# Kernel optimization log

Hardware: AMD Instinct MI355X
Metric: run time of the kernel (lower is better)

Reference implementation:

```python
import jax, jax.numpy as jnp
import numpy as np

E, M, K, INTER = 8, 4096, 2048, 5632
N = 2 * INTER  # gate + up projections fused in w1
TOPK = 2


def setup_inputs() -> dict:
    key = jax.random.key(0)
    k1, k2, k3, k4, k5 = jax.random.split(key, 5)
    a1 = jax.random.normal(k1, (M, K), dtype=jnp.float32)
    w1 = jax.random.normal(k2, (E, N, K), dtype=jnp.float32) * (K ** -0.5)
    w2 = jax.random.normal(k3, (E, K, INTER), dtype=jnp.float32) * (INTER ** -0.5)
    topk_weights = jax.random.uniform(k4, (M, TOPK), dtype=jnp.float32)
    topk_ids = jax.random.randint(k5, (M, TOPK), 0, E, dtype=jnp.int64)
    return {"a1": a1, "w1": w1, "w2": w2,
            "topk_weights": topk_weights, "topk_ids": topk_ids}


def reference(a1, w1, w2, topk_weights, topk_ids):
    # Fused MoE: dispatch (identity/unquantized path) -> per-expert
    # SwiGLU expert GEMMs -> weighted combine over top-k routing.
    n_half = w1.shape[1] // 2
    fused = jnp.zeros((a1.shape[0], topk_ids.shape[1], w2.shape[1]), a1.dtype)  # [M, topk, K]
    for e in range(w1.shape[0]):  # small fixed expert count
        h = jnp.einsum('mk,nk->mn', a1, w1[e])          # [M, N]
        act = jax.nn.silu(h[:, :n_half]) * h[:, n_half:]  # [M, N/2]
        o = jnp.einsum('mn,kn->mk', act, w2[e])          # [M, K]
        mask = (topk_ids == e).astype(a1.dtype)          # [M, topk]
        fused = fused + mask[..., None] * o[:, None, :]
    # combine: weighted reduction over topk -> output [M, K]
    return jnp.einsum('mt,mtk->mk', topk_weights, fused)
```

## Files before the change

### kernel.cpp

```cpp
#include <hip/hip_runtime.h>
#include <hip/hip_bf16.h>

#define NEXP   8
#define MTOK   4096
#define KDIM   2048
#define NINTER 5632
#define NPAIR  8192

#define AS3 __attribute__((address_space(3)))
#define AS1 __attribute__((address_space(1)))

typedef __attribute__((ext_vector_type(4))) float f32x4;
typedef __attribute__((ext_vector_type(8))) short s16x8;

__device__ __forceinline__ short f2bf(float f) {
  union { float f; unsigned u; } v; v.f = f;
  unsigned r = v.u + 0x7FFFu + ((v.u >> 16) & 1u);
  return (short)(r >> 16);
}

__device__ __forceinline__ s16x8 pack8(float4 a, float4 b) {
  s16x8 v;
  v[0] = f2bf(a.x); v[1] = f2bf(a.y); v[2] = f2bf(a.z); v[3] = f2bf(a.w);
  v[4] = f2bf(b.x); v[5] = f2bf(b.y); v[6] = f2bf(b.z); v[7] = f2bf(b.w);
  return v;
}

#define N8_A1  ((size_t)MTOK * KDIM / 8)
#define N8_W1  ((size_t)NEXP * 2 * NINTER * KDIM / 8)
__global__ __launch_bounds__(256) void routecvt_k(const int* __restrict__ ids,
                                                  int* __restrict__ off,
                                                  int* __restrict__ list,
                                                  const float* __restrict__ a1,
                                                  unsigned short* __restrict__ a1b,
                                                  const float* __restrict__ w1,
                                                  unsigned short* __restrict__ w1b) {
  int tid = threadIdx.x;
  if (blockIdx.x == 0) {
    __shared__ int sids[NPAIR];
    __shared__ int scnt[64][8];
    __shared__ int sstart[64][8];
    __shared__ int s_is64;
    if (tid == 0) s_is64 = 1;
    __syncthreads();
    for (int i = tid; i < NPAIR / 2; i += 256)
      if (ids[2 * i + 1] != 0) s_is64 = 0;
    __syncthreads();
    int is64 = s_is64;
    for (int i = tid; i < NPAIR; i += 256) {
      int e = is64 ? ids[2 * i] : ids[i];
      if (e < 0) e = 0; if (e > 7) e = 7;
      sids[i] = e;
    }
    if (tid < 64)
      for (int e = 0; e < 8; ++e) scnt[tid][e] = 0;
    __syncthreads();
    if (tid < 64) {
      int b0 = tid * 128;
      for (int i = 0; i < 128; ++i) ++scnt[tid][sids[b0 + i]];
    }
    __syncthreads();
    if (tid == 0) {
      int tot = 0;
      for (int e = 0; e < 8; ++e) {
        off[e] = tot;
        for (int c = 0; c < 64; ++c) { sstart[c][e] = tot; tot += scnt[c][e]; }
      }
      off[8] = tot;
    }
    __syncthreads();
    if (tid < 64) {
      int b0 = tid * 128;
      for (int i = 0; i < 128; ++i) {
        int p = b0 + i;
        int e = sids[p];
        list[sstart[tid][e]++] = p;
      }
    }
  }
  size_t i = (size_t)blockIdx.x * 256 + tid;
  size_t stride = (size_t)gridDim.x * 256;
  for (; i < N8_A1 + N8_W1; i += stride) {
    if (i < N8_A1) {
      const float4* p = (const float4*)(a1 + i * 8);
      float4 f0 = p[0], f1 = p[1];
      *(s16x8*)(a1b + i * 8) = pack8(f0, f1);
    } else {
      size_t j = i - N8_A1;
      const float4* p = (const float4*)(w1 + j * 8);
      float4 f0 = p[0], f1 = p[1];
      *(s16x8*)(w1b + j * 8) = pack8(f0, f1);
    }
  }
}

template <int BF>
__global__ __launch_bounds__(256, 2) void gemm1_t(const float* __restrict__ a1,
                                                  const unsigned short* __restrict__ a1b,
                                                  const float* __restrict__ w1,
                                                  const unsigned short* __restrict__ w1b,
                                                  const float* __restrict__ w2f,
                                                  unsigned short* __restrict__ w2b,
                                                  const int* __restrict__ off,
                                                  const int* __restrict__ list,
                                                  unsigned short* __restrict__ act) {
  int e = blockIdx.z, mt = blockIdx.y, nt = blockIdx.x;
  int tid = threadIdx.x;

  if constexpr (BF) {
    if (mt >= 64) {
      const size_t N8_W2 = (size_t)NEXP * KDIM * NINTER / 8;
      size_t ci = (size_t)nt + 44u * ((mt - 64) + 9u * e);
      size_t g0 = ci * 3642 + tid;
      size_t end = (ci + 1) * 3642;
      if (end > N8_W2) end = N8_W2;
      for (size_t g = g0; g < end; g += 256) {
        const float4* s = (const float4*)(w2f + g * 8);
        float4 f0 = s[0], f1 = s[1];
        *(s16x8*)(w2b + g * 8) = pack8(f0, f1);
      }
      return;
    }
  }

  int base = off[e];
  int cnt  = off[e + 1] - base;
  if (mt * 128 >= cnt) return;
  __shared__ __align__(16) short lA[128 * 64];
  __shared__ __align__(16) short lBg[128 * 64];
  __shared__ __align__(16) short lBu[128 * 64];
  __shared__ int srow[128];
  if (tid < 128) {
    int r = mt * 128 + tid;
    srow[tid] = (r < cnt) ? (list[base + r] >> 1) : 0;
  }
  __syncthreads();
  int lane = tid & 63, wave = tid >> 6;
  int wm = wave >> 1, wn = wave & 1;
  int lrow = lane & 15, lhi = lane >> 4;
  f32x4 accg[4][4], accu[4][4];
#pragma unroll
  for (int i = 0; i < 4; ++i)
#pragma unroll
    for (int j = 0; j < 4; ++j) { accg[i][j] = (f32x4)(0.f); accu[i][j] = (f32x4)(0.f); }
  int n0 = nt * 128;

  const unsigned short* aSrc[4];
  const unsigned short* gSrc[4];
  const unsigned short* uSrc[4];
  if constexpr (BF) {
    const unsigned short* w1be = w1b + (size_t)e * (2 * NINTER) * KDIM;
    int c = lane & 7;
#pragma unroll
    for (int q = 0; q < 4; ++q) {
      int r = wave * 32 + q * 8 + (lane >> 3);
      int swz = (c ^ (r & 7)) * 8;
      aSrc[q] = a1b + (size_t)srow[r] * KDIM + swz;
      gSrc[q] = w1be + (size_t)(n0 + r) * KDIM + swz;
      uSrc[q] = w1be + (size_t)(NINTER + n0 + r) * KDIM + swz;
    }
  }
  const float* w1e = w1 + (size_t)e * (2 * NINTER) * KDIM;

  for (int k0 = 0; k0 < KDIM; k0 += 64) {
    if constexpr (BF) {
#pragma unroll
      for (int q = 0; q < 4; ++q) {
        int row0 = wave * 32 + q * 8;
        __builtin_amdgcn_global_load_lds((const AS1 void*)(aSrc[q] + k0), (AS3 void*)&lA[row0 * 64], 16, 0, 0);
        __builtin_amdgcn_global_load_lds((const AS1 void*)(gSrc[q] + k0), (AS3 void*)&lBg[row0 * 64], 16, 0, 0);
        __builtin_amdgcn_global_load_lds((const AS1 void*)(uSrc[q] + k0), (AS3 void*)&lBu[row0 * 64], 16, 0, 0);
      }
    } else {
#pragma unroll
      for (int c4 = 0; c4 < 4; ++c4) {
        int cid = c4 * 256 + tid;
        int row = cid >> 3, k8 = cid & 7;
        const float* s = a1 + (size_t)srow[row] * KDIM + k0 + k8 * 8;
        float4 f0 = *(const float4*)s;
        float4 f1 = *(const float4*)(s + 4);
        *(s16x8*)&lA[row * 64 + ((k8 ^ (row & 7)) * 8)] = pack8(f0, f1);
      }
#pragma unroll
      for (int c4 = 0; c4 < 4; ++c4) {
        int cid = c4 * 256 + tid;
        int row = cid >> 3, k8 = cid & 7;
        const float* sg = w1e + (size_t)(n0 + row) * KDIM + k0 + k8 * 8;
        const float* su = w1e + (size_t)(NINTER + n0 + row) * KDIM + k0 + k8 * 8;
        float4 g0 = *(const float4*)sg;
        float4 g1 = *(const float4*)(sg + 4);
        float4 u0 = *(const float4*)su;
        float4 u1 = *(const float4*)(su + 4);
        int o = row * 64 + ((k8 ^ (row & 7)) * 8);
        *(s16x8*)&lBg[o] = pack8(g0, g1);
        *(s16x8*)&lBu[o] = pack8(u0, u1);
      }
    }
    __syncthreads();
#pragma unroll
    for (int kk = 0; kk < 2; ++kk) {
      s16x8 af[4], bg[4], bu[4];
      int chunk = kk * 4 + lhi;
#pragma unroll
      for (int i = 0; i < 4; ++i) {
        int r = wm * 64 + i * 16 + lrow;
        af[i] = *(const s16x8*)&lA[r * 64 + ((chunk ^ (r & 7)) * 8)];
      }
#pragma unroll
      for (int j = 0; j < 4; ++j) {
        int r = wn * 64 + j * 16 + lrow;
        int o = r * 64 + ((chunk ^ (r & 7)) * 8);
        bg[j] = *(const s16x8*)&lBg[o];
        bu[j] = *(const s16x8*)&lBu[o];
      }
#pragma unroll
      for (int i = 0; i < 4; ++i)
#pragma unroll
        for (int j = 0; j < 4; ++j) {
          accg[i][j] = __builtin_amdgcn_mfma_f32_16x16x32_bf16(af[i], bg[j], accg[i][j], 0, 0, 0);
          accu[i][j] = __builtin_amdgcn_mfma_f32_16x16x32_bf16(af[i], bu[j], accu[i][j], 0, 0, 0);
        }
    }
    __syncthreads();
  }
#pragma unroll
  for (int i = 0; i < 4; ++i) {
#pragma unroll
    for (int q = 0; q < 4; ++q) {
      int r = wm * 64 + i * 16 + lhi * 4 + q;
      int grow = mt * 128 + r;
      if (grow < cnt) {
        size_t rowoff = (size_t)(base + grow) * NINTER;
#pragma unroll
        for (int j = 0; j < 4; ++j) {
          float g = accg[i][j][q], u = accu[i][j][q];
          float a = (g / (1.f + __expf(-g))) * u;
          int col = n0 + wn * 64 + j * 16 + lrow;
          act[rowoff + col] = (unsigned short)f2bf(a);
        }
      }
    }
  }
}

template <int BF>
__global__ __launch_bounds__(256, 2) void gemm2_t(const unsigned short* __restrict__ act,
                                                  const float* __restrict__ w2,
                                                  const unsigned short* __restrict__ w2b,
                                                  const int* __restrict__ off,
                                                  const int* __restrict__ list,
                                                  const float* __restrict__ tw,
                                                  float* __restrict__ out) {
  int e = blockIdx.z, mt = blockIdx.y, nt = blockIdx.x;
  int base = off[e];
  int cnt  = off[e + 1] - base;
  if (mt * 128 >= cnt) return;
  __shared__ __align__(16) short lA[128 * 64];
  __shared__ __align__(16) short lB[128 * 64];
  int tid = threadIdx.x;
  int lane = tid & 63, wave = tid >> 6;
  int wm = wave >> 1, wn = wave & 1;
  int lrow = lane & 15, lhi = lane >> 4;
  f32x4 acc[4][4];
#pragma unroll
  for (int i = 0; i < 4; ++i)
#pragma unroll
    for (int j = 0; j < 4; ++j) acc[i][j] = (f32x4)(0.f);
  const float* w2e = w2 + (size_t)e * KDIM * NINTER;

  const unsigned short* aSrc[4];
  const unsigned short* bSrc[4];
  if constexpr (BF) {
    const unsigned short* w2be = w2b + (size_t)e * KDIM * NINTER;
    int c = lane & 7;
#pragma unroll
    for (int q = 0; q < 4; ++q) {
      int r = wave * 32 + q * 8 + (lane >> 3);
      int swz = (c ^ (r & 7)) * 8;
      int grow = mt * 128 + r;
      if (grow >= cnt) grow = cnt - 1;
      aSrc[q] = act + (size_t)(base + grow) * NINTER + swz;
      bSrc[q] = w2be + (size_t)(nt * 128 + r) * NINTER + swz;
    }
  }

  for (int k0 = 0; k0 < NINTER; k0 += 64) {
    if constexpr (BF) {
#pragma unroll
      for (int q = 0; q < 4; ++q) {
        int row0 = wave * 32 + q * 8;
        __builtin_amdgcn_global_load_lds((const AS1 void*)(aSrc[q] + k0), (AS3 void*)&lA[row0 * 64], 16, 0, 0);
        __builtin_amdgcn_global_load_lds((const AS1 void*)(bSrc[q] + k0), (AS3 void*)&lB[row0 * 64], 16, 0, 0);
      }
    } else {
#pragma unroll
      for (int c4 = 0; c4 < 4; ++c4) {
        int cid = c4 * 256 + tid;
        int row = cid >> 3, k8 = cid & 7;
        int grow = mt * 128 + row;
        if (grow >= cnt) grow = cnt - 1;
        s16x8 v = *(const s16x8*)(act + (size_t)(base + grow) * NINTER + k0 + k8 * 8);
        *(s16x8*)&lA[row * 64 + ((k8 ^ (row & 7)) * 8)] = v;
      }
#pragma unroll
      for (int c4 = 0; c4 < 4; ++c4) {
        int cid = c4 * 256 + tid;
        int row = cid >> 3, k8 = cid & 7;
        const float* s = w2e + (size_t)(nt * 128 + row) * NINTER + k0 + k8 * 8;
        float4 f0 = *(const float4*)s;
        float4 f1 = *(const float4*)(s + 4);
        *(s16x8*)&lB[row * 64 + ((k8 ^ (row & 7)) * 8)] = pack8(f0, f1);
      }
    }
    __syncthreads();
#pragma unroll
    for (int kk = 0; kk < 2; ++kk) {
      s16x8 af[4], bf[4];
      int chunk = kk * 4 + lhi;
#pragma unroll
      for (int i = 0; i < 4; ++i) {
        int r = wm * 64 + i * 16 + lrow;
        af[i] = *(const s16x8*)&lA[r * 64 + ((chunk ^ (r & 7)) * 8)];
      }
#pragma unroll
      for (int j = 0; j < 4; ++j) {
        int r = wn * 64 + j * 16 + lrow;
        bf[j] = *(const s16x8*)&lB[r * 64 + ((chunk ^ (r & 7)) * 8)];
      }
#pragma unroll
      for (int i = 0; i < 4; ++i)
#pragma unroll
        for (int j = 0; j < 4; ++j)
          acc[i][j] = __builtin_amdgcn_mfma_f32_16x16x32_bf16(af[i], bf[j], acc[i][j], 0, 0, 0);
    }
    __syncthreads();
  }
#pragma unroll
  for (int i = 0; i < 4; ++i) {
#pragma unroll
    for (int q = 0; q < 4; ++q) {
      int r = wm * 64 + i * 16 + lhi * 4 + q;
      int grow = mt * 128 + r;
      if (grow < cnt) {
        int p = list[base + grow];
        int m = p >> 1;
        float wgt = tw[p];
#pragma unroll
        for (int j = 0; j < 4; ++j) {
          int col = nt * 128 + wn * 64 + j * 16 + lrow;
          atomicAdd(&out[(size_t)m * KDIM + col], wgt * acc[i][j][q]);
        }
      }
    }
  }
}

__global__ __launch_bounds__(512) void route_k(const int* __restrict__ ids,
                                               int* __restrict__ off,
                                               int* __restrict__ list) {
  __shared__ int sids[NPAIR];
  __shared__ int scnt[64][8];
  __shared__ int sstart[64][8];
  __shared__ int s_is64;
  int tid = threadIdx.x;
  if (tid == 0) s_is64 = 1;
  __syncthreads();
  for (int i = tid; i < NPAIR / 2; i += 512)
    if (ids[2 * i + 1] != 0) s_is64 = 0;
  __syncthreads();
  int is64 = s_is64;
  for (int i = tid; i < NPAIR; i += 512) {
    int e = is64 ? ids[2 * i] : ids[i];
    if (e < 0) e = 0; if (e > 7) e = 7;
    sids[i] = e;
  }
  if (tid < 64)
    for (int e = 0; e < 8; ++e) scnt[tid][e] = 0;
  __syncthreads();
  if (tid < 64) {
    int b0 = tid * 128;
    for (int i = 0; i < 128; ++i) ++scnt[tid][sids[b0 + i]];
  }
  __syncthreads();
  if (tid == 0) {
    int tot = 0;
    for (int e = 0; e < 8; ++e) {
      off[e] = tot;
      for (int c = 0; c < 64; ++c) { sstart[c][e] = tot; tot += scnt[c][e]; }
    }
    off[8] = tot;
  }
  __syncthreads();
  if (tid < 64) {
    int b0 = tid * 128;
    for (int i = 0; i < 128; ++i) {
      int p = b0 + i;
      int e = sids[p];
      list[sstart[tid][e]++] = p;
    }
  }
}

extern "C" void kernel_launch(void* const* d_in, const int* in_sizes, int n_in,
                              void* d_out, int out_size, void* d_ws, size_t ws_size,
                              hipStream_t stream) {
  const float* a1 = (const float*)d_in[0];
  const float* w1 = (const float*)d_in[1];
  const float* w2 = (const float*)d_in[2];
  const float* tw = (const float*)d_in[3];
  const int*   ids = (const int*)d_in[4];
  float* out = (float*)d_out;

  int* off  = (int*)d_ws;
  int* list = off + 16;
  unsigned short* act = (unsigned short*)((char*)d_ws + 65536);
  size_t actB = (size_t)NPAIR * NINTER * 2;
  unsigned short* a1b = (unsigned short*)((char*)act + actB);
  size_t a1B = (size_t)MTOK * KDIM * 2;
  unsigned short* w1b = (unsigned short*)((char*)a1b + a1B);
  size_t w1B = (size_t)NEXP * 2 * NINTER * KDIM * 2;
  unsigned short* w2b = (unsigned short*)((char*)w1b + w1B);
  size_t w2B = (size_t)NEXP * KDIM * NINTER * 2;
  size_t need = 65536 + actB + a1B + w1B + w2B;

  hipMemsetAsync(d_out, 0, (size_t)MTOK * KDIM * sizeof(float), stream);

  if (ws_size >= need) {
    routecvt_k<<<4096, 256, 0, stream>>>(ids, off, list, a1, a1b, w1, w1b);
    gemm1_t<1><<<dim3(NINTER / 128, 73, NEXP), 256, 0, stream>>>(a1, a1b, w1, w1b, w2, w2b, off, list, act);
    gemm2_t<1><<<dim3(KDIM / 128, 64, NEXP), 256, 0, stream>>>(act, w2, w2b, off, list, tw, out);
  } else {
    route_k<<<1, 512, 0, stream>>>(ids, off, list);
    gemm1_t<0><<<dim3(NINTER / 128, 64, NEXP), 256, 0, stream>>>(a1, a1b, w1, w1b, w2, w2b, off, list, act);
    gemm2_t<0><<<dim3(KDIM / 128, 64, NEXP), 256, 0, stream>>>(act, w2, w2b, off, list, tw, out);
  }
}
```

Measured before the change: 1.006 ms.

## Fold w2 fp32-to-bf16 conversion into gemm1 k-loop of carrier blocks

Removes the dedicated extra grid rows (mt>=64) that converted w2 to bf16. The conversion is now spread across gemm1 blocks with mt<8: each converts 4096 chunks of 8 floats, one chunk every other k-step inside its main loop, or all at once if it has no tile to compute. The goal is to hide the memory-bound conversion behind the MFMA work and drop the extra blocks. The tradeoff is added global traffic and extra registers inside the GEMM inner loop of the carrier blocks.

```diff
diff --git a/kernel.cpp b/kernel.cpp
--- a/kernel.cpp
+++ b/kernel.cpp
@@ -106,26 +106,30 @@
                                                   unsigned short* __restrict__ act) {
   int e = blockIdx.z, mt = blockIdx.y, nt = blockIdx.x;
   int tid = threadIdx.x;
-
-  if constexpr (BF) {
-    if (mt >= 64) {
-      const size_t N8_W2 = (size_t)NEXP * KDIM * NINTER / 8;
-      size_t ci = (size_t)nt + 44u * ((mt - 64) + 9u * e);
-      size_t g0 = ci * 3642 + tid;
-      size_t end = (ci + 1) * 3642;
-      if (end > N8_W2) end = N8_W2;
-      for (size_t g = g0; g < end; g += 256) {
-        const float4* s = (const float4*)(w2f + g * 8);
-        float4 f0 = s[0], f1 = s[1];
-        *(s16x8*)(w2b + g * 8) = pack8(f0, f1);
-      }
-      return;
-    }
-  }
-
   int base = off[e];
   int cnt  = off[e + 1] - base;
-  if (mt * 128 >= cnt) return;
+
+  bool carrier = false;
+  size_t cb = 0;
+  if constexpr (BF) {
+    carrier = (mt < 8);
+    cb = ((size_t)nt + 44u * ((size_t)mt + 8u * (size_t)e)) * 4096;
+  }
+
+  if (mt * 128 >= cnt) {
+    if constexpr (BF) {
+      if (carrier) {
+        for (int s = 0; s < 16; ++s) {
+          size_t g = cb + (size_t)s * 256 + tid;
+          const float4* p = (const float4*)(w2f + g * 8);
+          float4 f0 = p[0], f1 = p[1];
+          *(s16x8*)(w2b + g * 8) = pack8(f0, f1);
+        }
+      }
+    }
+    return;
+  }
+
   __shared__ __align__(16) short lA[128 * 64];
   __shared__ __align__(16) short lBg[128 * 64];
   __shared__ __align__(16) short lBu[128 * 64];
@@ -170,6 +174,13 @@
         __builtin_amdgcn_global_load_lds((const AS1 void*)(aSrc[q] + k0), (AS3 void*)&lA[row0 * 64], 16, 0, 0);
         __builtin_amdgcn_global_load_lds((const AS1 void*)(gSrc[q] + k0), (AS3 void*)&lBg[row0 * 64], 16, 0, 0);
         __builtin_amdgcn_global_load_lds((const AS1 void*)(uSrc[q] + k0), (AS3 void*)&lBu[row0 * 64], 16, 0, 0);
+      }
+      int ks = k0 >> 6;
+      if (carrier && (ks & 1) == 0) {
+        size_t g = cb + (size_t)(ks >> 1) * 256 + tid;
+        const float4* p = (const float4*)(w2f + g * 8);
+        float4 f0 = p[0], f1 = p[1];
+        *(s16x8*)(w2b + g * 8) = pack8(f0, f1);
       }
     } else {
 #pragma unroll
@@ -427,7 +438,7 @@
 
   if (ws_size >= need) {
     routecvt_k<<<4096, 256, 0, stream>>>(ids, off, list, a1, a1b, w1, w1b);
-    gemm1_t<1><<<dim3(NINTER / 128, 73, NEXP), 256, 0, stream>>>(a1, a1b, w1, w1b, w2, w2b, off, list, act);
+    gemm1_t<1><<<dim3(NINTER / 128, 64, NEXP), 256, 0, stream>>>(a1, a1b, w1, w1b, w2, w2b, off, list, act);
     gemm2_t<1><<<dim3(KDIM / 128, 64, NEXP), 256, 0, stream>>>(act, w2, w2b, off, list, tw, out);
   } else {
     route_k<<<1, 512, 0, stream>>>(ids, off, list);
```

After: 998.2 us, median of 2. Within noise of the previous version (-0.8%).

## Load fp32 w2 tiles directly into LDS and convert to bf16 at fragment read

Applied to the files above, without the earlier changes.

Drops the separate fp32-to-bf16 conversion pass over w2 that ran as extra blocks inside gemm1. gemm2 now streams fp32 w2 tiles into LDS with async global-to-LDS loads and converts each fragment with the hardware packed bf16 convert instruction right before the MFMA. This saves a full read and write of w2 plus the bf16 copy's reread, but doubles w2 bytes fetched per tile and doubles the B tile's LDS footprint, which may reduce occupancy. Every M-tile rereads fp32 w2 and converts it again.

```diff
diff --git a/kernel.cpp b/kernel.cpp
--- a/kernel.cpp
+++ b/kernel.cpp
@@ -24,6 +24,15 @@
   v[0] = f2bf(a.x); v[1] = f2bf(a.y); v[2] = f2bf(a.z); v[3] = f2bf(a.w);
   v[4] = f2bf(b.x); v[5] = f2bf(b.y); v[6] = f2bf(b.z); v[7] = f2bf(b.w);
   return v;
+}
+
+__device__ __forceinline__ s16x8 cvtpk8(float4 a, float4 b) {
+  union { unsigned u[4]; s16x8 s; } r;
+  asm("v_cvt_pk_bf16_f32 %0, %1, %2" : "=v"(r.u[0]) : "v"(a.x), "v"(a.y));
+  asm("v_cvt_pk_bf16_f32 %0, %1, %2" : "=v"(r.u[1]) : "v"(a.z), "v"(a.w));
+  asm("v_cvt_pk_bf16_f32 %0, %1, %2" : "=v"(r.u[2]) : "v"(b.x), "v"(b.y));
+  asm("v_cvt_pk_bf16_f32 %0, %1, %2" : "=v"(r.u[3]) : "v"(b.z), "v"(b.w));
+  return r.s;
 }
 
 #define N8_A1  ((size_t)MTOK * KDIM / 8)
@@ -99,33 +108,15 @@
                                                   const unsigned short* __restrict__ a1b,
                                                   const float* __restrict__ w1,
                                                   const unsigned short* __restrict__ w1b,
-                                                  const float* __restrict__ w2f,
-                                                  unsigned short* __restrict__ w2b,
                                                   const int* __restrict__ off,
                                                   const int* __restrict__ list,
                                                   unsigned short* __restrict__ act) {
   int e = blockIdx.z, mt = blockIdx.y, nt = blockIdx.x;
   int tid = threadIdx.x;
-
-  if constexpr (BF) {
-    if (mt >= 64) {
-      const size_t N8_W2 = (size_t)NEXP * KDIM * NINTER / 8;
-      size_t ci = (size_t)nt + 44u * ((mt - 64) + 9u * e);
-      size_t g0 = ci * 3642 + tid;
-      size_t end = (ci + 1) * 3642;
-      if (end > N8_W2) end = N8_W2;
-      for (size_t g = g0; g < end; g += 256) {
-        const float4* s = (const float4*)(w2f + g * 8);
-        float4 f0 = s[0], f1 = s[1];
-        *(s16x8*)(w2b + g * 8) = pack8(f0, f1);
-      }
-      return;
-    }
-  }
-
   int base = off[e];
   int cnt  = off[e + 1] - base;
   if (mt * 128 >= cnt) return;
+
   __shared__ __align__(16) short lA[128 * 64];
   __shared__ __align__(16) short lBg[128 * 64];
   __shared__ __align__(16) short lBu[128 * 64];
@@ -244,9 +235,8 @@
 }
 
 template <int BF>
-__global__ __launch_bounds__(256, 2) void gemm2_t(const unsigned short* __restrict__ act,
+__global__ __launch_bounds__(256, 2) void gemm2_f(const unsigned short* __restrict__ act,
                                                   const float* __restrict__ w2,
-                                                  const unsigned short* __restrict__ w2b,
                                                   const int* __restrict__ off,
                                                   const int* __restrict__ list,
                                                   const float* __restrict__ tw,
@@ -256,7 +246,7 @@
   int cnt  = off[e + 1] - base;
   if (mt * 128 >= cnt) return;
   __shared__ __align__(16) short lA[128 * 64];
-  __shared__ __align__(16) short lB[128 * 64];
+  __shared__ __align__(16) float lB[128 * 64];
   int tid = threadIdx.x;
   int lane = tid & 63, wave = tid >> 6;
   int wm = wave >> 1, wn = wave & 1;
@@ -268,10 +258,18 @@
     for (int j = 0; j < 4; ++j) acc[i][j] = (f32x4)(0.f);
   const float* w2e = w2 + (size_t)e * KDIM * NINTER;
 
+  const float* bSrc[8];
+  int bDst[8];
+#pragma unroll
+  for (int q = 0; q < 8; ++q) {
+    int cid = q * 256 + tid;
+    int r = cid >> 4, c = cid & 15;
+    bSrc[q] = w2e + (size_t)(nt * 128 + r) * NINTER + ((c ^ (r & 7)) * 4);
+    bDst[q] = cid * 4;
+  }
+
   const unsigned short* aSrc[4];
-  const unsigned short* bSrc[4];
   if constexpr (BF) {
-    const unsigned short* w2be = w2b + (size_t)e * KDIM * NINTER;
     int c = lane & 7;
 #pragma unroll
     for (int q = 0; q < 4; ++q) {
@@ -280,7 +278,6 @@
       int grow = mt * 128 + r;
       if (grow >= cnt) grow = cnt - 1;
       aSrc[q] = act + (size_t)(base + grow) * NINTER + swz;
-      bSrc[q] = w2be + (size_t)(nt * 128 + r) * NINTER + swz;
     }
   }
 
@@ -290,7 +287,6 @@
       for (int q = 0; q < 4; ++q) {
         int row0 = wave * 32 + q * 8;
         __builtin_amdgcn_global_load_lds((const AS1 void*)(aSrc[q] + k0), (AS3 void*)&lA[row0 * 64], 16, 0, 0);
-        __builtin_amdgcn_global_load_lds((const AS1 void*)(bSrc[q] + k0), (AS3 void*)&lB[row0 * 64], 16, 0, 0);
       }
     } else {
 #pragma unroll
@@ -302,16 +298,10 @@
         s16x8 v = *(const s16x8*)(act + (size_t)(base + grow) * NINTER + k0 + k8 * 8);
         *(s16x8*)&lA[row * 64 + ((k8 ^ (row & 7)) * 8)] = v;
       }
-#pragma unroll
-      for (int c4 = 0; c4 < 4; ++c4) {
-        int cid = c4 * 256 + tid;
-        int row = cid >> 3, k8 = cid & 7;
-        const float* s = w2e + (size_t)(nt * 128 + row) * NINTER + k0 + k8 * 8;
-        float4 f0 = *(const float4*)s;
-        float4 f1 = *(const float4*)(s + 4);
-        *(s16x8*)&lB[row * 64 + ((k8 ^ (row & 7)) * 8)] = pack8(f0, f1);
-      }
-    }
+    }
+#pragma unroll
+    for (int q = 0; q < 8; ++q)
+      __builtin_amdgcn_global_load_lds((const AS1 void*)(bSrc[q] + k0), (AS3 void*)&lB[bDst[q]], 16, 0, 0);
     __syncthreads();
 #pragma unroll
     for (int kk = 0; kk < 2; ++kk) {
@@ -325,7 +315,10 @@
 #pragma unroll
       for (int j = 0; j < 4; ++j) {
         int r = wn * 64 + j * 16 + lrow;
-        bf[j] = *(const s16x8*)&lB[r * 64 + ((chunk ^ (r & 7)) * 8)];
+        int cc0 = (2 * chunk) ^ (r & 7), cc1 = (2 * chunk + 1) ^ (r & 7);
+        float4 f0 = *(const float4*)&lB[r * 64 + cc0 * 4];
+        float4 f1 = *(const float4*)&lB[r * 64 + cc1 * 4];
+        bf[j] = cvtpk8(f0, f1);
       }
 #pragma unroll
       for (int i = 0; i < 4; ++i)
@@ -419,19 +412,17 @@
   size_t a1B = (size_t)MTOK * KDIM * 2;
   unsigned short* w1b = (unsigned short*)((char*)a1b + a1B);
   size_t w1B = (size_t)NEXP * 2 * NINTER * KDIM * 2;
-  unsigned short* w2b = (unsigned short*)((char*)w1b + w1B);
-  size_t w2B = (size_t)NEXP * KDIM * NINTER * 2;
-  size_t need = 65536 + actB + a1B + w1B + w2B;
+  size_t need = 65536 + actB + a1B + w1B;
 
   hipMemsetAsync(d_out, 0, (size_t)MTOK * KDIM * sizeof(float), stream);
 
   if (ws_size >= need) {
     routecvt_k<<<4096, 256, 0, stream>>>(ids, off, list, a1, a1b, w1, w1b);
-    gemm1_t<1><<<dim3(NINTER / 128, 73, NEXP), 256, 0, stream>>>(a1, a1b, w1, w1b, w2, w2b, off, list, act);
-    gemm2_t<1><<<dim3(KDIM / 128, 64, NEXP), 256, 0, stream>>>(act, w2, w2b, off, list, tw, out);
+    gemm1_t<1><<<dim3(NINTER / 128, 64, NEXP), 256, 0, stream>>>(a1, a1b, w1, w1b, off, list, act);
+    gemm2_f<1><<<dim3(KDIM / 128, 64, NEXP), 256, 0, stream>>>(act, w2, off, list, tw, out);
   } else {
     route_k<<<1, 512, 0, stream>>>(ids, off, list);
-    gemm1_t<0><<<dim3(NINTER / 128, 64, NEXP), 256, 0, stream>>>(a1, a1b, w1, w1b, w2, w2b, off, list, act);
-    gemm2_t<0><<<dim3(KDIM / 128, 64, NEXP), 256, 0, stream>>>(act, w2, w2b, off, list, tw, out);
-  }
-}
+    gemm1_t<0><<<dim3(NINTER / 128, 64, NEXP), 256, 0, stream>>>(a1, a1b, w1, w1b, off, list, act);
+    gemm2_f<0><<<dim3(KDIM / 128, 64, NEXP), 256, 0, stream>>>(act, w2, off, list, tw, out);
+  }
+}
```

Result: no change. 1.007 ms (+0.1%).
